# Kernel tuning notes

Measured on AMD Instinct MI355X. Metric: run time of the kernel, lower is better.

## Reference

```python
import jax, jax.numpy as jnp
import numpy as np

EMB = 1024
H = 16
D = EMB // H  # 64
EPS = 1e-5
SM_SCALE = 1.0  # forward default sm_scale=1.0
CAUSAL = True
NEG = -1e30


def _layernorm(t, g, b):
    # LayerNorm over last dim (head_dim), per torch nn.LayerNorm(head_dim)
    m = jnp.mean(t, axis=-1, keepdims=True)
    v = jnp.mean(jnp.square(t - m), axis=-1, keepdims=True)
    return (t - m) * jax.lax.rsqrt(v + EPS) * g + b


def setup_inputs() -> dict:
    key = jax.random.key(0)
    ks = jax.random.split(key, 8)
    N, L = 2, 2048
    x = jax.random.normal(ks[0], (N, L, EMB), dtype=jnp.float32)
    mask = jnp.ones((N, L), dtype=jnp.int32)  # accepted but unused, as in the torch module
    s = 0.02
    Wq = jax.random.normal(ks[1], (EMB, EMB), dtype=jnp.float32) * s
    Wk = jax.random.normal(ks[2], (EMB, EMB), dtype=jnp.float32) * s
    Wv = jax.random.normal(ks[3], (EMB, EMB), dtype=jnp.float32) * s
    Wo = jax.random.normal(ks[4], (EMB, EMB), dtype=jnp.float32) * s
    bo = jnp.zeros((EMB,), dtype=jnp.float32)
    gq = jnp.ones((D,), dtype=jnp.float32)
    bq = jnp.zeros((D,), dtype=jnp.float32)
    gk = jnp.ones((D,), dtype=jnp.float32)
    bk = jnp.zeros((D,), dtype=jnp.float32)
    return {"x": x, "mask": mask, "Wq": Wq, "Wk": Wk, "Wv": Wv,
            "gq": gq, "bq": bq, "gk": gk, "bk": bk, "Wo": Wo, "bo": bo}


def reference(x, mask, Wq, Wk, Wv, gq, bq, gk, bk, Wo, bo):
    N, L, _ = x.shape
    # QKV projections (torch Linear: x @ W.T), split into heads -> [N, H, L, D]
    q = (x @ Wq.T).reshape(N, L, H, D).transpose(0, 2, 1, 3)
    k = (x @ Wk.T).reshape(N, L, H, D).transpose(0, 2, 1, 3)
    v = (x @ Wv.T).reshape(N, L, H, D).transpose(0, 2, 1, 3)
    # fused_q_norm variant: per-head LayerNorm on Q and K (fused into attention kernel)
    q = _layernorm(q, gq, bq)
    k = _layernorm(k, gk, bk)
    scores = jnp.einsum('nhld,nhmd->nhlm', q, k) * SM_SCALE  # [N,H,L,L]
    if CAUSAL:
        causal = jnp.tril(jnp.ones((L, L), dtype=bool))
        scores = jnp.where(causal, scores, NEG)
    attn = jax.nn.softmax(scores, axis=-1)
    out = jnp.einsum('nhlm,nhmd->nhld', attn, v)
    out = out.transpose(0, 2, 1, 3).reshape(N, L, EMB)
    return out @ Wo.T + bo
```

## Files before the change

kernel.cpp:

```cpp
#include <hip/hip_runtime.h>
#include <stdint.h>

typedef unsigned short u16;
typedef u16   u16x4    __attribute__((ext_vector_type(4)));
typedef u16   u16x8    __attribute__((ext_vector_type(8)));
typedef u16x8 u16x8_ma __attribute__((may_alias));
typedef __bf16 bf16x8  __attribute__((ext_vector_type(8)));
typedef float f32x4    __attribute__((ext_vector_type(4)));
typedef f32x4 f32x4_ma __attribute__((may_alias));

#define EMB    1024
#define NHEAD  16
#define HD     64
#define SEQ    2048
#define NBATCH 2
#define ROWS   (NBATCH*SEQ)
#define TSTRIDE 132

__device__ __forceinline__ u16 f2b(float f) {
  uint32_t u; __builtin_memcpy(&u, &f, 4);
  u = u + 0x7fffu + ((u >> 16) & 1u);
  return (u16)(u >> 16);
}
__device__ __forceinline__ u16x8 ld8(const u16* p) { return *(const u16x8_ma*)p; }
__device__ __forceinline__ void  st8(u16* p, u16x8 v) { *(u16x8_ma*)p = v; }
__device__ __forceinline__ bf16x8 asbf(u16x8 v) {
  union { u16x8 u; bf16x8 b; } c; c.u = v; return c.b;
}
__device__ __forceinline__ uint32_t cvtpk(float a, float b) {
  uint32_t r;
  asm("v_cvt_pk_bf16_f32 %0, %1, %2" : "=v"(r) : "v"(a), "v"(b));
  return r;
}
__device__ __forceinline__ void pl32swap(uint32_t &a, uint32_t &b) {
  asm("v_permlane32_swap_b32 %0, %1" : "+v"(a), "+v"(b));
}
__device__ __forceinline__ void pl16swap(uint32_t &a, uint32_t &b) {
  asm("v_permlane16_swap_b32 %0, %1" : "+v"(a), "+v"(b));
}
__device__ __forceinline__ void async_cp16(const u16* g, u16* l) {
  __builtin_amdgcn_global_load_lds(
      (const __attribute__((address_space(1))) void*)g,
      (__attribute__((address_space(3))) void*)l, 16, 0, 0);
}
__device__ __forceinline__ void xcd_swz(int gx, int gy, int &bx, int &by) {
  int lin = bx + gx * by;
  int q = (gx * gy) >> 3;
  int w = (lin & 7) * q + (lin >> 3);
  bx = w % gx; by = w / gx;
}

__global__ __launch_bounds__(256) void cvt_all(
    const float* __restrict__ x,
    const float* __restrict__ w0, const float* __restrict__ w1,
    const float* __restrict__ w2, const float* __restrict__ w3,
    u16* __restrict__ xd, u16* __restrict__ d0, u16* __restrict__ d1,
    u16* __restrict__ d2, u16* __restrict__ d3)
{
  int bid = blockIdx.x;
  const float* s; u16* d; int off;
  if (bid < 4096) { s = x; d = xd; off = bid; }
  else {
    int t = bid - 4096; int m = t >> 10; off = t & 1023;
    switch (m) {
      case 0: s = w0; d = d0; break;
      case 1: s = w1; d = d1; break;
      case 2: s = w2; d = d2; break;
      default: s = w3; d = d3; break;
    }
  }
  size_t i = ((size_t)off * 256 + threadIdx.x) * 4;
  f32x4 v = *(const f32x4_ma*)(s + i);
  u16x4 o;
  #pragma unroll
  for (int j = 0; j < 4; j++) o[j] = f2b(v[j]);
  *(u16x4*)(d + i) = o;
}

template<int AMODE>
__device__ __forceinline__ void gemm_acc_128x128(
    const u16* __restrict__ A, const u16* __restrict__ B,
    int m0, int n0, u16* As, u16* Bs, f32x4 acc[4][4])
{
  const int tid  = threadIdx.x;
  const int lane = tid & 63;
  const int wave = tid >> 6;
  const int wm   = (wave >> 1) * 64;
  const int wn   = (wave & 1) * 64;
  const int ar   = tid >> 2;
  const int ac   = (tid & 3) * 8;
  const int lm   = lane & 15;
  const int lk   = (lane >> 4) * 8;

  #pragma unroll
  for (int i = 0; i < 4; i++)
    #pragma unroll
    for (int j = 0; j < 4; j++)
      #pragma unroll
      for (int e = 0; e < 4; e++) acc[i][j][e] = 0.f;

  for (int k0 = 0; k0 < EMB; k0 += 64) {
    size_t a0[2], a1[2];
    #pragma unroll
    for (int pnl = 0; pnl < 2; pnl++) {
      int kc = k0 + pnl * 32 + ac;
      if (AMODE == 0) {
        a0[pnl] = (size_t)(m0 + ar)      * EMB + kc;
        a1[pnl] = (size_t)(m0 + ar + 64) * EMB + kc;
      } else {
        int h = kc >> 6, d = kc & 63;
        int r0 = m0 + ar, r1 = m0 + ar + 64;
        a0[pnl] = (((size_t)((r0 >> 11) * NHEAD + h)) * SEQ + (r0 & (SEQ-1))) * HD + d;
        a1[pnl] = (((size_t)((r1 >> 11) * NHEAD + h)) * SEQ + (r1 & (SEQ-1))) * HD + d;
      }
    }
    __syncthreads();
    #pragma unroll
    for (int pnl = 0; pnl < 2; pnl++) {
      const int pb = pnl * 4096;
      async_cp16(A + a0[pnl], As + pb + tid * 8);
      async_cp16(A + a1[pnl], As + pb + (tid + 256) * 8);
      async_cp16(B + (size_t)(n0 + ar)      * EMB + k0 + pnl * 32 + ac, Bs + pb + tid * 8);
      async_cp16(B + (size_t)(n0 + ar + 64) * EMB + k0 + pnl * 32 + ac, Bs + pb + (tid + 256) * 8);
    }
    __syncthreads();

    #pragma unroll
    for (int pnl = 0; pnl < 2; pnl++) {
      const int pb = pnl * 4096;
      bf16x8 af[4], bfr[4];
      #pragma unroll
      for (int i = 0; i < 4; i++)
        af[i] = asbf(ld8(As + pb + (wm + i * 16 + lm) * 32 + lk));
      #pragma unroll
      for (int j = 0; j < 4; j++)
        bfr[j] = asbf(ld8(Bs + pb + (wn + j * 16 + lm) * 32 + lk));
      #pragma unroll
      for (int i = 0; i < 4; i++)
        #pragma unroll
        for (int j = 0; j < 4; j++)
          acc[i][j] = __builtin_amdgcn_mfma_f32_16x16x32_bf16(af[i], bfr[j], acc[i][j], 0, 0, 0);
    }
  }
}

__device__ __forceinline__ void epilogue_scatter_ln(
    f32x4 acc[4][4], u16* dst, int m0, int n0, int head_base, int Hdst,
    const float* g, const float* b, int do_ln)
{
  const int lane = threadIdx.x & 63, wave = threadIdx.x >> 6;
  const int wm = (wave >> 1) * 64, wn = (wave & 1) * 64;
  const int lm = lane & 15, quad = lane >> 4;

  float gv[4], bv[4];
  #pragma unroll
  for (int j = 0; j < 4; j++) { gv[j] = g[j * 16 + lm]; bv[j] = b[j * 16 + lm]; }

  #pragma unroll
  for (int i = 0; i < 4; i++)
    #pragma unroll
    for (int r = 0; r < 4; r++) {
      float val[4];
      #pragma unroll
      for (int j = 0; j < 4; j++) val[j] = acc[i][j][r];
      if (do_ln) {
        float s = val[0] + val[1] + val[2] + val[3];
        #pragma unroll
        for (int o = 8; o >= 1; o >>= 1) s += __shfl_xor(s, o, 64);
        float mean = s * (1.f / 64.f);
        float ss = 0.f;
        #pragma unroll
        for (int j = 0; j < 4; j++) { val[j] -= mean; ss += val[j] * val[j]; }
        #pragma unroll
        for (int o = 8; o >= 1; o >>= 1) ss += __shfl_xor(ss, o, 64);
        float inv = rsqrtf(ss * (1.f / 64.f) + 1e-5f);
        #pragma unroll
        for (int j = 0; j < 4; j++) val[j] = val[j] * inv * gv[j] + bv[j];
      }
      int row = m0 + wm + i * 16 + quad * 4 + r;
      int bn = row >> 11, l = row & (SEQ - 1);
      #pragma unroll
      for (int j = 0; j < 4; j++) {
        int col = n0 + wn + j * 16 + lm;
        int hl = (col >> 6) - head_base, d = col & 63;
        dst[(((size_t)(bn * Hdst + hl)) * SEQ + l) * HD + d] = f2b(val[j]);
      }
    }
}

__device__ __forceinline__ void epilogue_transpose_v(
    f32x4 acc[4][4], u16* dst, int m0, int n0, int Hdst, u16* Ts)
{
  const int tid = threadIdx.x, lane = tid & 63, wave = tid >> 6;
  const int wm = (wave >> 1) * 64;
  const int lm = lane & 15, quad = lane >> 4;
  const int bn = m0 >> 11, l0 = m0 & (SEQ - 1);

  #pragma unroll
  for (int pass = 0; pass < 2; ++pass) {
    __syncthreads();
    if ((wave & 1) == pass) {
      #pragma unroll
      for (int i = 0; i < 4; i++)
        #pragma unroll
        for (int j = 0; j < 4; j++)
          #pragma unroll
          for (int r = 0; r < 4; r++)
            Ts[(j * 16 + lm) * TSTRIDE + wm + i * 16 + quad * 4 + r] =
                f2b(acc[i][j][r]);
    }
    __syncthreads();
    const int hl = (n0 >> 6) + pass;
    u16* base = dst + ((size_t)(bn * Hdst + hl)) * HD * SEQ + l0;
    #pragma unroll
    for (int it = 0; it < 4; ++it) {
      int e = it * 2048 + tid * 8;
      int d = e >> 7, l = e & 127;
      st8(base + (size_t)d * SEQ + l, ld8(Ts + d * TSTRIDE + l));
    }
  }
}

__global__ __launch_bounds__(256) void gemm_qk(
    const u16* __restrict__ x,
    const u16* __restrict__ Wq, const u16* __restrict__ Wk,
    const float* __restrict__ gq, const float* __restrict__ bq,
    const float* __restrict__ gk, const float* __restrict__ bk,
    u16* __restrict__ qd, u16* __restrict__ kb)
{
  __shared__ __align__(16) u16 As[128 * 64];
  __shared__ __align__(16) u16 Bs[128 * 64];
  int bx = blockIdx.x, by = blockIdx.y;
  xcd_swz(8, 32, bx, by);
  const int m0 = by * 128, n0 = bx * 128;
  f32x4 acc[4][4];
  if (blockIdx.z == 0) {
    gemm_acc_128x128<0>(x, Wq, m0, n0, As, Bs, acc);
    epilogue_scatter_ln(acc, qd, m0, n0, 0, NHEAD, gq, bq, 1);
  } else {
    gemm_acc_128x128<0>(x, Wk, m0, n0, As, Bs, acc);
    epilogue_scatter_ln(acc, kb, m0, n0, 0, NHEAD, gk, bk, 1);
  }
}

__global__ __launch_bounds__(256) void gemm_v(
    const u16* __restrict__ x, const u16* __restrict__ Wv,
    u16* __restrict__ vb)
{
  __shared__ __align__(16) u16 buf[128 * 64 * 2];
  u16* As = buf;
  u16* Bs = buf + 128 * 64;
  int bx = blockIdx.x, by = blockIdx.y;
  xcd_swz(8, 32, bx, by);
  const int m0 = by * 128, n0 = bx * 128;
  f32x4 acc[4][4];
  gemm_acc_128x128<0>(x, Wv, m0, n0, As, Bs, acc);
  epilogue_transpose_v(acc, vb, m0, n0, NHEAD, buf);
}

__global__ __launch_bounds__(256) void gemm_q(
    const u16* __restrict__ x, const u16* __restrict__ Wq,
    const float* __restrict__ gq, const float* __restrict__ bq,
    u16* __restrict__ qd)
{
  __shared__ __align__(16) u16 As[128 * 64];
  __shared__ __align__(16) u16 Bs[128 * 64];
  int bx = blockIdx.x, by = blockIdx.y;
  xcd_swz(8, 32, bx, by);
  const int m0 = by * 128, n0 = bx * 128;
  f32x4 acc[4][4];
  gemm_acc_128x128<0>(x, Wq, m0, n0, As, Bs, acc);
  epilogue_scatter_ln(acc, qd, m0, n0, 0, NHEAD, gq, bq, 1);
}
__global__ __launch_bounds__(256) void gemm_kv(
    const u16* __restrict__ x,
    const u16* __restrict__ Wk, const u16* __restrict__ Wv,
    const float* __restrict__ gk, const float* __restrict__ bk,
    u16* __restrict__ k, u16* __restrict__ v, int head_lo, int hpp)
{
  __shared__ __align__(16) u16 buf[128 * 64 * 2];
  u16* As = buf;
  u16* Bs = buf + 128 * 64;
  int bx = blockIdx.x, by = blockIdx.y;
  xcd_swz(hpp / 2, 32, bx, by);
  const int m0 = by * 128, n0 = bx * 128;
  const u16* W = (blockIdx.z == 0 ? Wk : Wv) + (size_t)head_lo * HD * EMB;
  f32x4 acc[4][4];
  gemm_acc_128x128<0>(x, W, m0, n0, As, Bs, acc);
  if (blockIdx.z == 0)
    epilogue_scatter_ln(acc, k, m0, n0, 0, hpp, gk, bk, 1);
  else
    epilogue_transpose_v(acc, v, m0, n0, hpp, buf);
}

__global__ __launch_bounds__(256, 4) void attn(
    u16* qd, const u16* __restrict__ K, const u16* __restrict__ V,
    int head_lo, int hpp)
{
  __shared__ __align__(16) u16 Ks[2][64 * 64];
  __shared__ __align__(16) u16 Vt[2][64 * 64];

  int p, hl, n;
  if (hpp == NHEAD) {
    const int lin = blockIdx.x + 32 * (blockIdx.y + NHEAD * blockIdx.z);
    const int xcd = lin & 7, idx = lin >> 3;
    const int slot = idx & 3, pp = idx >> 2;
    const int hi = pp >> 3, lo = pp & 7;
    p = (hi & 1) ? (hi * 8 + 7 - lo) : (hi * 8 + lo);
    const int head = xcd * 4 + slot;
    n = head >> 4; hl = head & 15;
  } else {
    hl = blockIdx.y; n = blockIdx.z;
    const int perm = (7 * blockIdx.x + (hl & 7) + 8 * n) & 31;
    p = perm ^ (31 * (hl >> 3));
  }
  const int tid = threadIdx.x, lane = tid & 63, wave = tid >> 6;
  const int lm = lane & 15, quad = lane >> 4;
  u16* Qh = qd + ((size_t)(n * NHEAD + head_lo + hl)) * SEQ * HD;
  const u16* Kh = K + ((size_t)(n * hpp + hl)) * SEQ * HD;
  const u16* Vh = V + ((size_t)(n * hpp + hl)) * HD * SEQ;

  const int c0 = tid, c1 = tid + 256;
  const int kk0 = c0 >> 3, kd0 = ((c0 & 7) ^ (kk0 & 7)) * 8;
  const int kk1 = c1 >> 3, kd1 = ((c1 & 7) ^ (kk1 & 7)) * 8;
  const int vd0 = kk0, vg0 = kd0;
  const int vd1 = kk1, vg1 = kd1;

  const int lk = quad * 8;
  bf16x8 aq[2];
  #pragma unroll
  for (int ks = 0; ks < 2; ++ks)
    aq[ks] = asbf(ld8(Qh + (size_t)(p * 64 + wave * 16 + lm) * HD + ks * 32 + lk));

  #define STAGE(buf, t)                                                        \
    {                                                                          \
      const u16* Kt = Kh + (size_t)(t) * 64 * HD;                              \
      const u16* Vg = Vh + (size_t)(t) * 64;                                   \
      async_cp16(Kt + (size_t)kk0 * HD + kd0, &Ks[buf][0] + tid * 8);          \
      async_cp16(Kt + (size_t)kk1 * HD + kd1, &Ks[buf][0] + (tid + 256) * 8);  \
      async_cp16(Vg + (size_t)vd0 * SEQ + vg0, &Vt[buf][0] + tid * 8);         \
      async_cp16(Vg + (size_t)vd1 * SEQ + vg1, &Vt[buf][0] + (tid + 256) * 8); \
    }

  STAGE(0, 0);
  __syncthreads();

  f32x4 oacc[4];
  #pragma unroll
  for (int j = 0; j < 4; j++)
    #pragma unroll
    for (int e = 0; e < 4; e++) oacc[j][e] = 0.f;
  float m_i = -1e30f, psum = 0.f;

  const int qrow = p * 64 + wave * 16 + lm;
  const int xh = lm & 7;

  for (int t = 0; t <= p; ++t) {
    const int cur = t & 1;
    if (t < p) STAGE(1 - cur, t + 1);

    f32x4 s[4];
    #pragma unroll
    for (int j = 0; j < 4; j++)
      #pragma unroll
      for (int e = 0; e < 4; e++) s[j][e] = 0.f;
    __builtin_amdgcn_s_setprio(1);
    #pragma unroll
    for (int ks = 0; ks < 2; ++ks)
      #pragma unroll
      for (int j = 0; j < 4; j++) {
        bf16x8 ak = asbf(ld8(&Ks[cur][((j * 16 + lm) << 6) +
                                      (((ks * 4 + quad) ^ xh) << 3)]));
        s[j] = __builtin_amdgcn_mfma_f32_16x16x32_bf16(ak, aq[ks], s[j], 0, 0, 0);
      }
    __builtin_amdgcn_s_setprio(0);

    if (t == p) {
      #pragma unroll
      for (int j = 0; j < 4; j++)
        #pragma unroll
        for (int r = 0; r < 4; r++)
          if (t * 64 + j * 16 + quad * 4 + r > qrow) s[j][r] = -1e30f;
    }

    float mx = fmaxf(fmaxf(s[0][0], s[0][1]), fmaxf(s[0][2], s[0][3]));
    #pragma unroll
    for (int j = 1; j < 4; j++)
      mx = fmaxf(mx, fmaxf(fmaxf(s[j][0], s[j][1]), fmaxf(s[j][2], s[j][3])));
    mx = fmaxf(mx, __shfl_xor(mx, 16, 64));
    mx = fmaxf(mx, __shfl_xor(mx, 32, 64));

    const bool defer = __all(mx <= m_i + 8.f);
    float alpha = 1.f;
    if (!defer) {
      const float mnew = fmaxf(m_i, mx);
      alpha = __expf(m_i - mnew);
      m_i = mnew;
    }
    float part = 0.f;
    #pragma unroll
    for (int j = 0; j < 4; j++)
      #pragma unroll
      for (int r = 0; r < 4; r++) {
        float pv = __expf(s[j][r] - m_i);
        s[j][r] = pv;
        part += pv;
      }
    if (defer) {
      psum += part;
    } else {
      psum = psum * alpha + part;
      float ar_[4];
      #pragma unroll
      for (int r = 0; r < 4; r++)
        ar_[r] = __shfl(alpha, (lane & 48) | (quad * 4 + r), 64);
      #pragma unroll
      for (int j = 0; j < 4; j++)
        #pragma unroll
        for (int r = 0; r < 4; r++) oacc[j][r] *= ar_[r];
    }

    uint32_t u[8];
    #pragma unroll
    for (int j = 0; j < 4; j++) {
      u[2 * j]     = cvtpk(s[j][0], s[j][1]);
      u[2 * j + 1] = cvtpk(s[j][2], s[j][3]);
    }

    __builtin_amdgcn_s_setprio(1);
    #pragma unroll
    for (int ks = 0; ks < 2; ++ks) {
      uint32_t a0 = u[ks * 4 + 0], a1 = u[ks * 4 + 1];
      uint32_t a2 = u[ks * 4 + 2], a3 = u[ks * 4 + 3];
      pl32swap(a0, a2);
      pl16swap(a0, a2);
      pl32swap(a1, a3);
      pl16swap(a1, a3);
      union { uint32_t w[4]; bf16x8 v; } cv;
      cv.w[0] = a0; cv.w[1] = a1; cv.w[2] = a2; cv.w[3] = a3;
      bf16x8 ap = cv.v;
      #pragma unroll
      for (int j = 0; j < 4; j++) {
        bf16x8 bv = asbf(ld8(&Vt[cur][((j * 16 + lm) << 6) +
                                      (((ks * 4 + quad) ^ xh) << 3)]));
        oacc[j] = __builtin_amdgcn_mfma_f32_16x16x32_bf16(ap, bv, oacc[j], 0, 0, 0);
      }
    }
    __builtin_amdgcn_s_setprio(0);
    __syncthreads();
  }
  #undef STAGE

  float s_ = psum;
  s_ += __shfl_xor(s_, 16, 64);
  s_ += __shfl_xor(s_, 32, 64);
  const float inv = 1.0f / s_;
  float ir_[4];
  #pragma unroll
  for (int r = 0; r < 4; r++)
    ir_[r] = __shfl(inv, (lane & 48) | (quad * 4 + r), 64);
  #pragma unroll
  for (int r = 0; r < 4; r++) {
    const int row = p * 64 + wave * 16 + quad * 4 + r;
    #pragma unroll
    for (int j = 0; j < 4; j++)
      Qh[(size_t)row * HD + j * 16 + lm] = f2b(oacc[j][r] * ir_[r]);
  }
}

__global__ __launch_bounds__(256) void gemm_out(
    const u16* __restrict__ ao, const u16* __restrict__ Wo,
    const float* __restrict__ bo, float* __restrict__ out)
{
  __shared__ __align__(16) u16 As[64 * 64];
  __shared__ __align__(16) u16 Bs[128 * 64];
  int bx = blockIdx.x, by = blockIdx.y;
  xcd_swz(8, 64, bx, by);
  const int m0 = by * 64, n0 = bx * 128;
  const int tid  = threadIdx.x;
  const int lane = tid & 63;
  const int wave = tid >> 6;
  const int wm   = (wave >> 1) * 32;
  const int wn   = (wave & 1) * 64;
  const int ar   = tid >> 2;
  const int ac   = (tid & 3) * 8;
  const int lm   = lane & 15;
  const int lk   = (lane >> 4) * 8;

  f32x4 acc[2][4];
  #pragma unroll
  for (int i = 0; i < 2; i++)
    #pragma unroll
    for (int j = 0; j < 4; j++)
      #pragma unroll
      for (int e = 0; e < 4; e++) acc[i][j][e] = 0.f;

  for (int k0 = 0; k0 < EMB; k0 += 64) {
    size_t aoff[2];
    #pragma unroll
    for (int pnl = 0; pnl < 2; pnl++) {
      int kc = k0 + pnl * 32 + ac, h = kc >> 6, d = kc & 63;
      int r0 = m0 + ar;
      aoff[pnl] = (((size_t)((r0 >> 11) * NHEAD + h)) * SEQ + (r0 & (SEQ-1))) * HD + d;
    }
    __syncthreads();
    #pragma unroll
    for (int pnl = 0; pnl < 2; pnl++) {
      async_cp16(ao + aoff[pnl], As + pnl * 2048 + tid * 8);
      async_cp16(Wo + (size_t)(n0 + ar)      * EMB + k0 + pnl * 32 + ac, Bs + pnl * 4096 + tid * 8);
      async_cp16(Wo + (size_t)(n0 + ar + 64) * EMB + k0 + pnl * 32 + ac, Bs + pnl * 4096 + (tid + 256) * 8);
    }
    __syncthreads();

    #pragma unroll
    for (int pnl = 0; pnl < 2; pnl++) {
      bf16x8 af[2], bfr[4];
      #pragma unroll
      for (int i = 0; i < 2; i++)
        af[i] = asbf(ld8(As + pnl * 2048 + (wm + i * 16 + lm) * 32 + lk));
      #pragma unroll
      for (int j = 0; j < 4; j++)
        bfr[j] = asbf(ld8(Bs + pnl * 4096 + (wn + j * 16 + lm) * 32 + lk));
      #pragma unroll
      for (int i = 0; i < 2; i++)
        #pragma unroll
        for (int j = 0; j < 4; j++)
          acc[i][j] = __builtin_amdgcn_mfma_f32_16x16x32_bf16(af[i], bfr[j], acc[i][j], 0, 0, 0);
    }
  }

  const int quad = lane >> 4;
  #pragma unroll
  for (int j = 0; j < 4; j++) {
    int col = n0 + wn + j * 16 + lm;
    float bias = bo[col];
    #pragma unroll
    for (int i = 0; i < 2; i++)
      #pragma unroll
      for (int r = 0; r < 4; r++) {
        int row = m0 + wm + i * 16 + quad * 4 + r;
        out[(size_t)row * EMB + col] = acc[i][j][r] + bias;
      }
  }
}

extern "C" void kernel_launch(void* const* d_in, const int* in_sizes, int n_in,
                              void* d_out, int out_size, void* d_ws, size_t ws_size,
                              hipStream_t stream)
{
  const float* xf  = (const float*)d_in[0];
  const float* Wqf = (const float*)d_in[2];
  const float* Wkf = (const float*)d_in[3];
  const float* Wvf = (const float*)d_in[4];
  const float* gq  = (const float*)d_in[5];
  const float* bq  = (const float*)d_in[6];
  const float* gk  = (const float*)d_in[7];
  const float* bk  = (const float*)d_in[8];
  const float* Wof = (const float*)d_in[9];
  const float* bo  = (const float*)d_in[10];

  const size_t MB = 1u << 20;
  u16* xb  = (u16*)d_ws;
  u16* wqb = xb  + (size_t)ROWS * EMB;
  u16* wkb = wqb + (size_t)EMB * EMB;
  u16* wvb = wkb + (size_t)EMB * EMB;
  u16* wob = wvb + (size_t)EMB * EMB;
  u16* kvbase = wob + (size_t)EMB * EMB;

  size_t avail = (ws_size > 16 * MB) ? ws_size - 16 * MB : 2 * MB;
  int hpp = NHEAD;
  while ((size_t)hpp * MB > avail && hpp > 2) hpp >>= 1;
  const size_t kv_elems = (size_t)hpp * NBATCH * SEQ * HD;
  u16* kbuf = kvbase;
  u16* vbuf = kbuf + kv_elems;

  u16* qd = (u16*)d_in[0];
  float* out = (float*)d_out;

  cvt_all<<<dim3(8192), 256, 0, stream>>>(xf, Wqf, Wkf, Wvf, Wof,
                                          xb, wqb, wkb, wvb, wob);
  if (hpp == NHEAD) {
    gemm_qk<<<dim3(8, 32, 2), 256, 0, stream>>>(xb, wqb, wkb,
                                                gq, bq, gk, bk, qd, kbuf);
    gemm_v<<<dim3(8, 32), 256, 0, stream>>>(xb, wvb, vbuf);
    attn<<<dim3(32, NHEAD, NBATCH), 256, 0, stream>>>(qd, kbuf, vbuf, 0, NHEAD);
  } else {
    gemm_q<<<dim3(8, 32), 256, 0, stream>>>(xb, wqb, gq, bq, qd);
    for (int g = 0; g < NHEAD / hpp; ++g) {
      gemm_kv<<<dim3(hpp / 2, 32, 2), 256, 0, stream>>>(xb, wkb, wvb, gk, bk,
                                                        kbuf, vbuf, g * hpp, hpp);
      attn<<<dim3(32, hpp, NBATCH), 256, 0, stream>>>(qd, kbuf, vbuf, g * hpp, hpp);
    }
  }
  gemm_out<<<dim3(8, 64), 256, 0, stream>>>(qd, wob, bo, out);
}
```

Before: 200.3 us.

## Software-pipeline attention PV matmul one tile behind QK with triple-buffered V

The P·V MFMA for tile t-1 is deferred into iteration t and issued right after the QK^T MFMAs, so matrix work can overlap with the softmax math instead of waiting on it. V gets a third LDS buffer so the deferred tile stays valid while the next tile is staged, and a final PV step runs after the loop. The row-max reduction is also rebuilt as a tree of 3-input max operations. The cost is more LDS per block and the packed P fragments kept live across iterations, which may add register pressure.

```diff
diff --git a/kernel.cpp b/kernel.cpp
--- a/kernel.cpp
+++ b/kernel.cpp
@@ -37,6 +37,9 @@
 }
 __device__ __forceinline__ void pl16swap(uint32_t &a, uint32_t &b) {
   asm("v_permlane16_swap_b32 %0, %1" : "+v"(a), "+v"(b));
+}
+__device__ __forceinline__ float m3(float a, float b, float c) {
+  return fmaxf(fmaxf(a, b), c);
 }
 __device__ __forceinline__ void async_cp16(const u16* g, u16* l) {
   __builtin_amdgcn_global_load_lds(
@@ -298,7 +301,7 @@
     int head_lo, int hpp)
 {
   __shared__ __align__(16) u16 Ks[2][64 * 64];
-  __shared__ __align__(16) u16 Vt[2][64 * 64];
+  __shared__ __align__(16) u16 Vt[3][64 * 64];
 
   int p, hl, n;
   if (hpp == NHEAD) {
@@ -323,8 +326,6 @@
   const int c0 = tid, c1 = tid + 256;
   const int kk0 = c0 >> 3, kd0 = ((c0 & 7) ^ (kk0 & 7)) * 8;
   const int kk1 = c1 >> 3, kd1 = ((c1 & 7) ^ (kk1 & 7)) * 8;
-  const int vd0 = kk0, vg0 = kd0;
-  const int vd1 = kk1, vg1 = kd1;
 
   const int lk = quad * 8;
   bf16x8 aq[2];
@@ -332,17 +333,21 @@
   for (int ks = 0; ks < 2; ++ks)
     aq[ks] = asbf(ld8(Qh + (size_t)(p * 64 + wave * 16 + lm) * HD + ks * 32 + lk));
 
-  #define STAGE(buf, t)                                                        \
+  #define STAGEK(buf, t)                                                       \
     {                                                                          \
       const u16* Kt = Kh + (size_t)(t) * 64 * HD;                              \
-      const u16* Vg = Vh + (size_t)(t) * 64;                                   \
       async_cp16(Kt + (size_t)kk0 * HD + kd0, &Ks[buf][0] + tid * 8);          \
       async_cp16(Kt + (size_t)kk1 * HD + kd1, &Ks[buf][0] + (tid + 256) * 8);  \
-      async_cp16(Vg + (size_t)vd0 * SEQ + vg0, &Vt[buf][0] + tid * 8);         \
-      async_cp16(Vg + (size_t)vd1 * SEQ + vg1, &Vt[buf][0] + (tid + 256) * 8); \
-    }
-
-  STAGE(0, 0);
+    }
+  #define STAGEV(buf, t)                                                       \
+    {                                                                          \
+      const u16* Vg = Vh + (size_t)(t) * 64;                                   \
+      async_cp16(Vg + (size_t)kk0 * SEQ + kd0, &Vt[buf][0] + tid * 8);         \
+      async_cp16(Vg + (size_t)kk1 * SEQ + kd1, &Vt[buf][0] + (tid + 256) * 8); \
+    }
+
+  STAGEK(0, 0);
+  STAGEV(0, 0);
   __syncthreads();
 
   f32x4 oacc[4];
@@ -351,13 +356,17 @@
     #pragma unroll
     for (int e = 0; e < 4; e++) oacc[j][e] = 0.f;
   float m_i = -1e30f, psum = 0.f;
+  bf16x8 pa0, pa1;
 
   const int qrow = p * 64 + wave * 16 + lm;
   const int xh = lm & 7;
 
   for (int t = 0; t <= p; ++t) {
-    const int cur = t & 1;
-    if (t < p) STAGE(1 - cur, t + 1);
+    const int kcur = t & 1;
+    if (t < p) {
+      STAGEK(1 - kcur, t + 1);
+      STAGEV((t + 1) % 3, t + 1);
+    }
 
     f32x4 s[4];
     #pragma unroll
@@ -369,10 +378,22 @@
     for (int ks = 0; ks < 2; ++ks)
       #pragma unroll
       for (int j = 0; j < 4; j++) {
-        bf16x8 ak = asbf(ld8(&Ks[cur][((j * 16 + lm) << 6) +
-                                      (((ks * 4 + quad) ^ xh) << 3)]));
+        bf16x8 ak = asbf(ld8(&Ks[kcur][((j * 16 + lm) << 6) +
+                                       (((ks * 4 + quad) ^ xh) << 3)]));
         s[j] = __builtin_amdgcn_mfma_f32_16x16x32_bf16(ak, aq[ks], s[j], 0, 0, 0);
       }
+    if (t > 0) {
+      const u16* Vb = &Vt[(t + 2) % 3][0];
+      #pragma unroll
+      for (int ks = 0; ks < 2; ++ks)
+        #pragma unroll
+        for (int j = 0; j < 4; j++) {
+          bf16x8 bv = asbf(ld8(Vb + ((j * 16 + lm) << 6) +
+                                    (((ks * 4 + quad) ^ xh) << 3)));
+          oacc[j] = __builtin_amdgcn_mfma_f32_16x16x32_bf16(
+              ks == 0 ? pa0 : pa1, bv, oacc[j], 0, 0, 0);
+        }
+    }
     __builtin_amdgcn_s_setprio(0);
 
     if (t == p) {
@@ -383,10 +404,12 @@
           if (t * 64 + j * 16 + quad * 4 + r > qrow) s[j][r] = -1e30f;
     }
 
-    float mx = fmaxf(fmaxf(s[0][0], s[0][1]), fmaxf(s[0][2], s[0][3]));
-    #pragma unroll
-    for (int j = 1; j < 4; j++)
-      mx = fmaxf(mx, fmaxf(fmaxf(s[j][0], s[j][1]), fmaxf(s[j][2], s[j][3])));
+    float g1 = m3(s[0][0], s[0][1], s[0][2]);
+    float g2 = m3(s[0][3], s[1][0], s[1][1]);
+    float g3 = m3(s[1][2], s[1][3], s[2][0]);
+    float g4 = m3(s[2][1], s[2][2], s[2][3]);
+    float g5 = m3(s[3][0], s[3][1], s[3][2]);
+    float mx = fmaxf(m3(g1, g2, g3), m3(g4, g5, s[3][3]));
     mx = fmaxf(mx, __shfl_xor(mx, 16, 64));
     mx = fmaxf(mx, __shfl_xor(mx, 32, 64));
 
@@ -426,8 +449,6 @@
       u[2 * j]     = cvtpk(s[j][0], s[j][1]);
       u[2 * j + 1] = cvtpk(s[j][2], s[j][3]);
     }
-
-    __builtin_amdgcn_s_setprio(1);
     #pragma unroll
     for (int ks = 0; ks < 2; ++ks) {
       uint32_t a0 = u[ks * 4 + 0], a1 = u[ks * 4 + 1];
@@ -438,18 +459,27 @@
       pl16swap(a1, a3);
       union { uint32_t w[4]; bf16x8 v; } cv;
       cv.w[0] = a0; cv.w[1] = a1; cv.w[2] = a2; cv.w[3] = a3;
-      bf16x8 ap = cv.v;
+      if (ks == 0) pa0 = cv.v; else pa1 = cv.v;
+    }
+    __syncthreads();
+  }
+
+  {
+    const u16* Vb = &Vt[p % 3][0];
+    __builtin_amdgcn_s_setprio(1);
+    #pragma unroll
+    for (int ks = 0; ks < 2; ++ks)
       #pragma unroll
       for (int j = 0; j < 4; j++) {
-        bf16x8 bv = asbf(ld8(&Vt[cur][((j * 16 + lm) << 6) +
-                                      (((ks * 4 + quad) ^ xh) << 3)]));
-        oacc[j] = __builtin_amdgcn_mfma_f32_16x16x32_bf16(ap, bv, oacc[j], 0, 0, 0);
+        bf16x8 bv = asbf(ld8(Vb + ((j * 16 + lm) << 6) +
+                                  (((ks * 4 + quad) ^ xh) << 3)));
+        oacc[j] = __builtin_amdgcn_mfma_f32_16x16x32_bf16(
+            ks == 0 ? pa0 : pa1, bv, oacc[j], 0, 0, 0);
       }
-    }
     __builtin_amdgcn_s_setprio(0);
-    __syncthreads();
-  }
-  #undef STAGE
+  }
+  #undef STAGEK
+  #undef STAGEV
 
   float s_ = psum;
   s_ += __shfl_xor(s_, 16, 64);
```

Measured after the change: 199.2 us. Within noise of the previous version (-0.5%).
